# Kernel tuning notes

Measured on AMD Instinct MI355X. Metric: run time of the kernel, lower is better.

The kernel has to match this reference:

```python
import jax, jax.numpy as jnp
import numpy as np

B = 1024
D = 128  # in_out_dim


def _lin(k, i, o):
    return jax.random.normal(k, (i, o), jnp.float32) / np.sqrt(i)


def setup_inputs() -> dict:
    key = jax.random.key(0)
    ks = jax.random.split(key, 24)
    inp = {
        'pseudo_t': jax.random.uniform(ks[0], (), jnp.float32),
        'x': jax.random.normal(ks[1], (B, D), jnp.float32),
        'g_x': jax.random.normal(ks[2], (B, 1), jnp.float32),
        'p': jax.random.uniform(ks[3], (B, 1), jnp.float32),
        # GRN encoder: 128->1024->960->896 (Tanh), decoder 896->128
        'gw0': _lin(ks[4], 128, 1024), 'gb0': jnp.zeros((1024,), jnp.float32),
        'gw1': _lin(ks[5], 1024, 960), 'gb1': jnp.zeros((960,), jnp.float32),
        'gw2': _lin(ks[6], 960, 896), 'gb2': jnp.zeros((896,), jnp.float32),
        'gdw': _lin(ks[7], 896, 128), 'gdb': jnp.zeros((128,), jnp.float32),
        # BRD encoder: 129->512->448 (Tanh), decoder 448->1
        'bw0': _lin(ks[8], 129, 512), 'bb0': jnp.zeros((512,), jnp.float32),
        'bw1': _lin(ks[9], 512, 448), 'bb1': jnp.zeros((448,), jnp.float32),
        'bdw': _lin(ks[10], 448, 1), 'bdb': jnp.zeros((1,), jnp.float32),
    }
    return inp


def reference(pseudo_t, x, g_x, p, gw0, gb0, gw1, gb1, gw2, gb2, gdw, gdb,
              bw0, bb0, bw1, bb1, bdw, bdb):
    bsz = x.shape[0]
    x_gene = x[:, :-1]                       # [B, D-1]
    s = jnp.full((bsz, 1), pseudo_t, x.dtype)

    def grn(state):                          # [..., D] -> [..., D]
        h = jnp.tanh(state @ gw0 + gb0)
        h = jnp.tanh(h @ gw1 + gb1)
        h = jnp.tanh(h @ gw2 + gb2)
        return h @ gdw + gdb

    dx_dt = grn(jnp.concatenate([s, x_gene], axis=1))   # [B, D]

    # BRD growth function g(x, t)
    st = jnp.concatenate([s, x], axis=1)                # [B, D+1]
    e = jnp.tanh(st @ bw0 + bb0)
    e = jnp.tanh(e @ bw1 + bb1)
    g = e @ bdw + bdb                                   # [B, 1]

    # trace of d(dx_dt[:, :D-1]) / d(x_gene), per sample (CNF divergence)
    s_scalar = jnp.reshape(pseudo_t, (1,)).astype(x.dtype)

    def f_single(xg_i):                                 # [D-1] -> [D]
        return grn(jnp.concatenate([s_scalar, xg_i]))

    jac = jax.vmap(jax.jacfwd(f_single))(x_gene)        # [B, D, D-1]
    tr = jnp.trace(jac[:, :D - 1, :], axis1=1, axis2=2) # [B]

    dp_dt = g - p * tr[:, None]                         # [B, 1]
    return (dx_dt, g, dp_dt)
```

## Files before the change

kernel.cpp:

```cpp
#include <hip/hip_runtime.h>


typedef __bf16 bf16;
typedef __bf16 bf16x8 __attribute__((ext_vector_type(8)));
typedef float floatx4 __attribute__((ext_vector_type(4)));

#if defined(__has_builtin)
#if __has_builtin(__builtin_amdgcn_global_load_lds)
#define HAVE_GLL 1
#endif
#endif

typedef __attribute__((address_space(3))) char lds_char_t;
typedef __attribute__((address_space(1))) const char gbl_char_t;

__device__ inline void async_load16(const void* gp, void* lp) {
#ifdef HAVE_GLL
  __builtin_amdgcn_global_load_lds((gbl_char_t*)gp, (lds_char_t*)lp, 16, 0, 0);
#else
  *(bf16x8*)lp = *(const bf16x8*)gp;
#endif
}

__device__ inline void stage_async(const bf16* src, long row0, int ld, int kc,
                                   bf16* dst, int wid, int sr8, int cph) {
#pragma unroll
  for (int t = 0; t < 4; ++t) {
    const int r = (wid * 4 + t) * 8 + sr8;
    const int csrc = (cph - r) & 7;
    async_load16(src + (row0 + r) * (size_t)ld + kc + csrc * 8,
                 dst + r * 64 + cph * 8);
  }
}

__device__ inline void mfma_block(const bf16* As, const bf16* Bs,
                                  floatx4 (&acc)[4][4], int wm, int wn,
                                  int l16, int quad) {
#pragma unroll
  for (int ks = 0; ks < 2; ++ks) {
    bf16x8 af[4], bfv[4];
#pragma unroll
    for (int mt = 0; mt < 4; ++mt) {
      const int r = wm * 64 + mt * 16 + l16;
      const int c = (ks * 4 + quad + r) & 7;
      af[mt] = *(const bf16x8*)(As + r * 64 + c * 8);
    }
#pragma unroll
    for (int nt = 0; nt < 4; ++nt) {
      const int r = wn * 64 + nt * 16 + l16;
      const int c = (ks * 4 + quad + r) & 7;
      bfv[nt] = *(const bf16x8*)(Bs + r * 64 + c * 8);
    }
#pragma unroll
    for (int mt = 0; mt < 4; ++mt)
#pragma unroll
      for (int nt = 0; nt < 4; ++nt)
        acc[mt][nt] = __builtin_amdgcn_mfma_f32_16x16x32_bf16(af[mt], bfv[nt], acc[mt][nt], 0, 0, 0);
  }
}

__device__ inline void g0_body(bf16* G0, const bf16* gw0b, const bf16* d0b,
                               int i0, int ch, int b, int tid) {
  const int nb = ((b >> 9) << 3) + (b & 7);
  const int inner = (b >> 3) & 63;
  if (nb >= ch) return;
  const int e = inner * 256 + tid;
  const int d = e >> 7;
  const int j = (e & 127) << 3;
  const int ig = i0 + nb;
  const int wsel = (d + 1 < 128) ? d + 1 : 127;
  bf16x8 gv = *(const bf16x8*)(gw0b + wsel * 1024 + j);
  bf16x8 dv = *(const bf16x8*)(d0b + (size_t)ig * 1024 + j);
  bf16x8 v;
#pragma unroll
  for (int k = 0; k < 8; ++k) v[k] = (bf16)((float)gv[k] * (float)dv[k]);
  *(bf16x8*)(G0 + ((size_t)nb * 128 + d) * 1024 + j) = v;
}

struct TArgs {
  const bf16* A;
  const bf16* B;
  const bf16* d1b;
  bf16* Upr;
  const bf16* d2b;
  const float* gdw;
  float* tr;
  int i0; int K; int ch;
};

__global__ __launch_bounds__(256, 4) void kt_b1(TArgs p) {
  const int idx = blockIdx.x;
  const int mt8 = (idx >> 3) & 7;
  const int nb  = ((idx >> 6) << 3) + (idx & 7);
  if (nb >= p.ch) return;

  __shared__ __align__(16) char lds[34816];
  bf16* As = (bf16*)lds;
  bf16* Bs = As + 8192;
  bf16* bounce = (bf16*)lds;

  const int tid  = threadIdx.x;
  const int wid  = tid >> 6, lane = tid & 63;
  const int wm   = wid & 1, wn = wid >> 1;
  const int quad = lane >> 4, l16 = lane & 15;
  const int sr8  = lane >> 3, cph = lane & 7;
  const int m0   = mt8 * 128;
  const int ig   = p.i0 + nb;
  const int n0   = nb * 128;

  floatx4 acc[4][4];
#pragma unroll
  for (int a = 0; a < 4; ++a)
#pragma unroll
    for (int b = 0; b < 4; ++b)
#pragma unroll
      for (int r = 0; r < 4; ++r) acc[a][b][r] = 0.0f;

  for (int kc = 0; kc < p.K; kc += 64) {
    stage_async(p.A, m0, 1024, kc, As, wid, sr8, cph);
    stage_async(p.B, n0, 1024, kc, Bs, wid, sr8, cph);
    __syncthreads();
    mfma_block(As, Bs, acc, wm, wn, l16, quad);
    __syncthreads();
  }

#pragma unroll
  for (int nt = 0; nt < 4; ++nt) {
    const int nl = wn * 64 + nt * 16 + l16;
#pragma unroll
    for (int mt = 0; mt < 4; ++mt)
#pragma unroll
      for (int r = 0; r < 4; ++r) {
        const int ml = wm * 64 + mt * 16 + quad * 4 + r;
        const int mg = m0 + ml;
        const float d1v = (mg < 960) ? (float)p.d1b[(size_t)ig * 960 + mg] : 0.0f;
        bounce[nl * 136 + ml] = (bf16)(acc[mt][nt][r] * d1v);
      }
  }
  __syncthreads();
  const int r2 = tid >> 1, half16 = tid & 1;
  const int chLim = (mt8 == 7) ? 8 : 16;
#pragma unroll
  for (int c = 0; c < 8; ++c) {
    const int ch16 = half16 * 8 + c;
    if (ch16 < chLim) {
      bf16x8 v = *(const bf16x8*)(bounce + r2 * 136 + ch16 * 8);
      *(bf16x8*)(p.Upr + (size_t)(n0 + r2) * 1024 + m0 + ch16 * 8) = v;
    }
  }
}

__global__ __launch_bounds__(256, 4) void kt_b2g0(TArgs p, int nB2,
                                                  bf16* G0n, const bf16* gw0b,
                                                  const bf16* d0b, int i0n, int chn) {
  __shared__ __align__(16) char lds[34816];
  __shared__ float red4[4];
  const int tid = threadIdx.x;
  const int idx = blockIdx.x;

  if (idx >= nB2) {
    if (chn > 0) g0_body(G0n, gw0b, d0b, i0n, chn, idx - nB2, tid);
    return;
  }

  const int mt8 = (idx >> 3) & 7;
  const int nb  = ((idx >> 6) << 3) + (idx & 7);
  if (nb >= p.ch || mt8 == 7) return;

  bf16* As = (bf16*)lds;
  bf16* Bs = As + 8192;

  const int wid  = tid >> 6, lane = tid & 63;
  const int wm   = wid & 1, wn = wid >> 1;
  const int quad = lane >> 4, l16 = lane & 15;
  const int sr8  = lane >> 3, cph = lane & 7;
  const int m0   = mt8 * 128;
  const int ig   = p.i0 + nb;
  const int n0   = nb * 128;

  floatx4 acc[4][4];
#pragma unroll
  for (int a = 0; a < 4; ++a)
#pragma unroll
    for (int b = 0; b < 4; ++b)
#pragma unroll
      for (int r = 0; r < 4; ++r) acc[a][b][r] = 0.0f;

  for (int kc = 0; kc < p.K; kc += 64) {
    stage_async(p.A, m0, 1024, kc, As, wid, sr8, cph);
    stage_async(p.B, n0, 1024, kc, Bs, wid, sr8, cph);
    __syncthreads();
    mfma_block(As, Bs, acc, wm, wn, l16, quad);
    __syncthreads();
  }

  float s = 0.0f;
#pragma unroll
  for (int nt = 0; nt < 4; ++nt) {
    const int d = wn * 64 + nt * 16 + l16;
    if (d < 127) {
#pragma unroll
      for (int mt = 0; mt < 4; ++mt)
#pragma unroll
        for (int r = 0; r < 4; ++r) {
          const int mg = m0 + wm * 64 + mt * 16 + quad * 4 + r;
          const float w = (float)p.d2b[(size_t)ig * 896 + mg] * p.gdw[mg * 128 + d];
          s += acc[mt][nt][r] * w;
        }
    }
  }
#pragma unroll
  for (int off = 1; off < 64; off <<= 1) s += __shfl_xor(s, off, 64);
  if (lane == 0) red4[wid] = s;
  __syncthreads();
  if (tid == 0) atomicAdd(p.tr + ig, red4[0] + red4[1] + red4[2] + red4[3]);
}

struct FArgs {
  const bf16* A; int lda;
  const bf16* Bt; int ldb;
  const float* bias;
  bf16* C; int ldc;
  bf16* D; int ldd;
  float* outF; int ldo;
  int K; int realN; int gridX;
};

template <int ACT>
__device__ inline void fwd_body(const FArgs& p, int bx, bf16* As, bf16* Bs) {
  const int tid  = threadIdx.x;
  const int wid  = tid >> 6, lane = tid & 63;
  const int wm   = wid & 1, wn = wid >> 1;
  const int quad = lane >> 4, l16 = lane & 15;
  const int sr8  = lane >> 3, cph = lane & 7;
  const int m0   = (bx % p.gridX) * 128;
  const int bn0  = (bx / p.gridX) * 128;

  floatx4 acc[4][4];
#pragma unroll
  for (int a = 0; a < 4; ++a)
#pragma unroll
    for (int b = 0; b < 4; ++b)
#pragma unroll
      for (int r = 0; r < 4; ++r) acc[a][b][r] = 0.0f;

  for (int kc = 0; kc < p.K; kc += 64) {
    stage_async(p.A, m0, p.lda, kc, As, wid, sr8, cph);
    stage_async(p.Bt, bn0, p.ldb, kc, Bs, wid, sr8, cph);
    __syncthreads();
    mfma_block(As, Bs, acc, wm, wn, l16, quad);
    __syncthreads();
  }

#pragma unroll
  for (int nt = 0; nt < 4; ++nt) {
    const int ng = bn0 + wn * 64 + nt * 16 + l16;
    const float bv = (ng < p.realN) ? p.bias[ng] : 0.0f;
#pragma unroll
    for (int mt = 0; mt < 4; ++mt)
#pragma unroll
      for (int r = 0; r < 4; ++r) {
        const int i = m0 + wm * 64 + mt * 16 + quad * 4 + r;
        const float v = acc[mt][nt][r] + bv;
        if (ACT) {
          const float t = tanhf(v);
          p.C[(size_t)i * p.ldc + ng] = (ng < p.realN) ? (bf16)t : (bf16)0.0f;
          if (p.D && ng < p.realN)
            p.D[(size_t)i * p.ldd + ng] = (bf16)(1.0f - t * t);
        } else if (ng < p.realN) {
          p.outF[(size_t)i * p.ldo + ng] = v;
        }
      }
  }
}

__global__ __launch_bounds__(256) void kt_fwd2(FArgs a, int na, FArgs b) {
  __shared__ __align__(16) bf16 As[8192];
  __shared__ __align__(16) bf16 Bs[8192];
  const int bx = blockIdx.x;
  if (bx < na) fwd_body<1>(a, bx, As, Bs);
  else         fwd_body<1>(b, bx - na, As, Bs);
}

__global__ __launch_bounds__(256) void kt_l2g0(FArgs a, int na, bf16* G0,
                                               const bf16* gw0b, const bf16* d0b,
                                               int i0, int ch) {
  __shared__ __align__(16) bf16 As[8192];
  __shared__ __align__(16) bf16 Bs[8192];
  const int bx = blockIdx.x;
  if (bx < na) fwd_body<1>(a, bx, As, Bs);
  else         g0_body(G0, gw0b, d0b, i0, ch, bx - na, threadIdx.x);
}

__global__ __launch_bounds__(256) void kt_dxgdot(FArgs a, int na,
                                                 const bf16* e1b, const float* bdw,
                                                 const float* bdb, float* gf,
                                                 float* gout) {
  __shared__ __align__(16) bf16 As[8192];
  __shared__ __align__(16) bf16 Bs[8192];
  const int bx = blockIdx.x;
  if (bx < na) { fwd_body<0>(a, bx, As, Bs); return; }
  const int i = (bx - na) * 4 + (threadIdx.x >> 6);
  const int lane = threadIdx.x & 63;
  float s = 0.0f;
  for (int k = lane; k < 448; k += 64) s += (float)e1b[(size_t)i * 512 + k] * bdw[k];
#pragma unroll
  for (int off = 32; off > 0; off >>= 1) s += __shfl_down(s, off, 64);
  if (lane == 0) {
    const float v = s + bdb[0];
    gf[i] = v;
    gout[i] = v;
  }
}

struct PArgs {
  const float *gw0, *gw1, *gw2, *gdw, *bw0, *bw1, *pt, *x;
  bf16 *gw0b, *gw0t, *gw1t, *gw2t, *gdwt, *bw0t, *bw1t, *Xg, *Xb;
};

__device__ inline void tpose_tile(bf16* dst, const float* src, int R, int C,
                                  int ldd, int tile, int tilesX, float* tl,
                                  int tid) {
  const int r0 = (tile % tilesX) * 64;
  const int c0 = (tile / tilesX) * 64;
  const int tx = tid & 63, ty0 = tid >> 6;
#pragma unroll
  for (int i = 0; i < 16; ++i) {
    const int ty = ty0 + i * 4;
    const int r = r0 + ty, c = c0 + tx;
    tl[ty * 65 + tx] = (r < R && c < C) ? src[(size_t)r * C + c] : 0.0f;
  }
  __syncthreads();
#pragma unroll
  for (int i = 0; i < 16; ++i) {
    const int ty = ty0 + i * 4;
    dst[(size_t)(c0 + ty) * ldd + r0 + tx] = (bf16)tl[tx * 65 + ty];
  }
}

__global__ __launch_bounds__(256) void kt_prep(PArgs p) {
  __shared__ float tl[64 * 65];
  int b = blockIdx.x;
  const int t = threadIdx.x;
  if (b < 512) { p.gw0b[b * 256 + t] = (bf16)p.gw0[b * 256 + t]; return; }
  b -= 512;
  if (b < 768) {
    const int idx = b * 256 + t;
    const int i = idx / 192, c = idx % 192;
    const float s = p.pt[0];
    float vb;
    if (c == 0) vb = s;
    else if (c <= 128) vb = p.x[i * 128 + c - 1];
    else vb = 0.0f;
    p.Xb[i * 192 + c] = (bf16)vb;
    if (c < 128) p.Xg[i * 128 + c] = (bf16)((c == 0) ? s : p.x[i * 128 + c - 1]);
    return;
  }
  b -= 768;
  if (b < 32)  { tpose_tile(p.gw0t, p.gw0, 128, 1024, 128, b, 2, tl, t);  return; }
  b -= 32;
  if (b < 256) { tpose_tile(p.gw1t, p.gw1, 1024, 960, 1024, b, 16, tl, t); return; }
  b -= 256;
  if (b < 256) { tpose_tile(p.gw2t, p.gw2, 960, 896, 1024, b, 16, tl, t); return; }
  b -= 256;
  if (b < 32)  { tpose_tile(p.gdwt, p.gdw, 896, 128, 1024, b, 16, tl, t); return; }
  b -= 32;
  if (b < 24)  { tpose_tile(p.bw0t, p.bw0, 129, 512, 192, b, 3, tl, t);  return; }
  b -= 24;
  if (b < 64)  { tpose_tile(p.bw1t, p.bw1, 512, 448, 512, b, 8, tl, t);  return; }
}

__global__ __launch_bounds__(256) void kt_fin(const float* gf, const float* tr,
                                              const float* pp, float* dp) {
  const int i = blockIdx.x * 256 + threadIdx.x;
  if (i < 1024) dp[i] = gf[i] - pp[i] * tr[i];
}

extern "C" void kernel_launch(void* const* d_in, const int* in_sizes, int n_in,
                              void* d_out, int out_size, void* d_ws, size_t ws_size,
                              hipStream_t stream) {
  const float* pt  = (const float*)d_in[0];
  const float* x   = (const float*)d_in[1];
  const float* pp  = (const float*)d_in[3];
  const float* gw0 = (const float*)d_in[4];
  const float* gb0 = (const float*)d_in[5];
  const float* gw1 = (const float*)d_in[6];
  const float* gb1 = (const float*)d_in[7];
  const float* gw2 = (const float*)d_in[8];
  const float* gb2 = (const float*)d_in[9];
  const float* gdw = (const float*)d_in[10];
  const float* gdb = (const float*)d_in[11];
  const float* bw0 = (const float*)d_in[12];
  const float* bb0 = (const float*)d_in[13];
  const float* bw1 = (const float*)d_in[14];
  const float* bb1 = (const float*)d_in[15];
  const float* bdw = (const float*)d_in[16];
  const float* bdb = (const float*)d_in[17];
  float* out = (float*)d_out;

  char* w = (char*)d_ws;
  size_t used = 0;
  auto alloc = [&](size_t nbytes) -> void* {
    void* r = w + used;
    used += (nbytes + 255) & ~(size_t)255;
    return r;
  };
  bf16* gw0b = (bf16*)alloc((size_t)128 * 1024 * 2);
  bf16* gw0t = (bf16*)alloc((size_t)1024 * 128 * 2);
  bf16* gw1t = (bf16*)alloc((size_t)1024 * 1024 * 2);
  bf16* gw2t = (bf16*)alloc((size_t)1024 * 1024 * 2);
  bf16* gdwt = (bf16*)alloc((size_t)128 * 1024 * 2);
  bf16* bw0t = (bf16*)alloc((size_t)512 * 192 * 2);
  bf16* bw1t = (bf16*)alloc((size_t)512 * 512 * 2);
  bf16* Xg   = (bf16*)alloc((size_t)1024 * 128 * 2);
  bf16* Xb   = (bf16*)alloc((size_t)1024 * 192 * 2);
  bf16* h0b  = (bf16*)alloc((size_t)1024 * 1024 * 2);
  bf16* h1b  = (bf16*)alloc((size_t)1024 * 1024 * 2);
  bf16* h2b  = (bf16*)alloc((size_t)1024 * 1024 * 2);
  bf16* e0b  = (bf16*)alloc((size_t)1024 * 512 * 2);
  bf16* e1b  = (bf16*)alloc((size_t)1024 * 512 * 2);
  bf16* d0b  = (bf16*)alloc((size_t)1024 * 1024 * 2);
  bf16* d1b  = (bf16*)alloc((size_t)1024 * 960 * 2);
  bf16* d2b  = (bf16*)alloc((size_t)1024 * 896 * 2);
  float* gf  = (float*)alloc(1024 * 4);
  float* tr  = (float*)alloc(1024 * 4);

  const size_t perSample = (size_t)128 * 1024 * 2;
  size_t avail = (ws_size > used) ? ws_size - used : 0;
  int CH = (int)(avail / (2 * perSample));
  if (CH > 256) CH = 256;
  if (CH < 1) CH = 1;
  bf16* G0  = (bf16*)alloc((size_t)CH * perSample);
  bf16* Upr = (bf16*)(w + used);

  hipMemsetAsync(tr, 0, 1024 * 4, stream);

  {
    PArgs a{gw0, gw1, gw2, gdw, bw0, bw1, pt, x,
            gw0b, gw0t, gw1t, gw2t, gdwt, bw0t, bw1t, Xg, Xb};
    kt_prep<<<dim3(1944), 256, 0, stream>>>(a);
  }

  {
    FArgs a{}; a.A = Xg; a.lda = 128; a.Bt = gw0t; a.ldb = 128; a.bias = gb0;
    a.C = h0b; a.ldc = 1024; a.D = d0b; a.ldd = 1024; a.K = 128; a.realN = 1024;
    a.gridX = 8;
    FArgs b{}; b.A = Xb; b.lda = 192; b.Bt = bw0t; b.ldb = 192; b.bias = bb0;
    b.C = e0b; b.ldc = 512; b.K = 192; b.realN = 512; b.gridX = 8;
    kt_fwd2<<<dim3(96), 256, 0, stream>>>(a, 64, b);
  }
  {
    FArgs a{}; a.A = h0b; a.lda = 1024; a.Bt = gw1t; a.ldb = 1024; a.bias = gb1;
    a.C = h1b; a.ldc = 1024; a.D = d1b; a.ldd = 960; a.K = 1024; a.realN = 960;
    a.gridX = 8;
    FArgs b{}; b.A = e0b; b.lda = 512; b.Bt = bw1t; b.ldb = 512; b.bias = bb1;
    b.C = e1b; b.ldc = 512; b.K = 512; b.realN = 448; b.gridX = 8;
    kt_fwd2<<<dim3(96), 256, 0, stream>>>(a, 64, b);
  }
  const int ch0  = (1024 < CH) ? 1024 : CH;
  const int ch08 = (ch0 + 7) & ~7;
  {
    FArgs a{}; a.A = h1b; a.lda = 1024; a.Bt = gw2t; a.ldb = 1024; a.bias = gb2;
    a.C = h2b; a.ldc = 1024; a.D = d2b; a.ldd = 896; a.K = 1024; a.realN = 896;
    a.gridX = 8;
    kt_l2g0<<<dim3(56 + ch08 * 64), 256, 0, stream>>>(a, 56, G0, gw0b, d0b, 0, ch0);
  }
  {
    FArgs a{}; a.A = h2b; a.lda = 1024; a.Bt = gdwt; a.ldb = 1024; a.bias = gdb;
    a.outF = out; a.ldo = 128; a.K = 896; a.realN = 128; a.gridX = 8;
    kt_dxgdot<<<dim3(8 + 256), 256, 0, stream>>>(a, 8, e1b, bdw, bdb, gf, out + 131072);
  }

  for (int i0 = 0; i0 < 1024; i0 += CH) {
    const int ch  = (1024 - i0 < CH) ? (1024 - i0) : CH;
    const int ch8 = (ch + 7) & ~7;
    {
      TArgs a{}; a.A = gw1t; a.B = G0; a.d1b = d1b; a.Upr = Upr; a.i0 = i0;
      a.K = 1024; a.ch = ch;
      kt_b1<<<dim3(8 * ch8), 256, 0, stream>>>(a);
    }
    {
      const int i0n = i0 + CH;
      const int chn = (i0n < 1024) ? ((1024 - i0n < CH) ? (1024 - i0n) : CH) : 0;
      const int chn8 = (chn + 7) & ~7;
      TArgs a{}; a.A = gw2t; a.B = Upr; a.d2b = d2b; a.gdw = gdw; a.tr = tr;
      a.i0 = i0; a.K = 960; a.ch = ch;
      kt_b2g0<<<dim3(8 * ch8 + chn8 * 64), 256, 0, stream>>>(
          a, 8 * ch8, G0, gw0b, d0b, i0n, chn);
    }
  }

  kt_fin<<<dim3(4), 256, 0, stream>>>(gf, tr, pp, out + 132096);
}
```

Before: 840.4 us.

## Replace Jacobian GEMM kernels with 256x256-tile double-buffered pipelined MFMA kernels

The two per-chunk Jacobian GEMMs move from 128x128 tiles with 256 threads and a synchronous single-buffer K loop to 256x256 tiles with 512 threads. The new K loop uses 128KB of dynamic LDS, a double-buffered async global-to-LDS prefetch with swizzled layout, explicit vmcnt waits and setprio around the MFMA bursts. The epilogue writes directly to global memory instead of bouncing through LDS. The next-chunk G0 construction changes from extra appended blocks to a grid-stride loop run by all GEMM blocks after their tile. This targets higher arithmetic intensity and overlap of loads with MFMA, at the cost of fewer resident blocks and wave-quantization effects on the larger tiles.

```diff
diff --git a/kernel.cpp b/kernel.cpp
--- a/kernel.cpp
+++ b/kernel.cpp
@@ -77,143 +77,221 @@
   *(bf16x8*)(G0 + ((size_t)nb * 128 + d) * 1024 + j) = v;
 }
 
-struct TArgs {
+struct T8 {
   const bf16* A;
-  const bf16* B;
-  const bf16* d1b;
+  const bf16* Bm;
+  const bf16* sc;
   bf16* Upr;
-  const bf16* d2b;
   const float* gdw;
   float* tr;
-  int i0; int K; int ch;
+  int i0, NT, ch, nTiles;
+  int chn, i0n;
+  bf16* G0;
+  const bf16* gw0b;
+  const bf16* d0b;
 };
 
-__global__ __launch_bounds__(256, 4) void kt_b1(TArgs p) {
-  const int idx = blockIdx.x;
-  const int mt8 = (idx >> 3) & 7;
-  const int nb  = ((idx >> 6) << 3) + (idx & 7);
-  if (nb >= p.ch) return;
-
-  __shared__ __align__(16) char lds[34816];
-  bf16* As = (bf16*)lds;
-  bf16* Bs = As + 8192;
-  bf16* bounce = (bf16*)lds;
-
-  const int tid  = threadIdx.x;
-  const int wid  = tid >> 6, lane = tid & 63;
-  const int wm   = wid & 1, wn = wid >> 1;
+__device__ __forceinline__ void gemm256(const bf16* Aop, const bf16* Bop,
+                                        int m0, int n0, int NT, char* lds,
+                                        floatx4 (&acc)[8][4]) {
+  const int tid = threadIdx.x;
+  const int wid = tid >> 6, lane = tid & 63;
+  const int wm = wid & 1, wn = wid >> 1;
   const int quad = lane >> 4, l16 = lane & 15;
-  const int sr8  = lane >> 3, cph = lane & 7;
-  const int m0   = mt8 * 128;
-  const int ig   = p.i0 + nb;
-  const int n0   = nb * 128;
-
-  floatx4 acc[4][4];
-#pragma unroll
-  for (int a = 0; a < 4; ++a)
+
+  const int sr = tid >> 2;
+  const int sg = tid & 3;
+  const int gs = sg ^ (sr & 3);
+  const bf16* aS0 = Aop + (size_t)(m0 + sr) * 1024 + gs * 8;
+  const bf16* aS1 = aS0 + (size_t)128 * 1024;
+  const bf16* bS0 = Bop + (size_t)(n0 + sr) * 1024 + gs * 8;
+  const bf16* bS1 = bS0 + (size_t)128 * 1024;
+  const int dO0 = tid * 16, dO1 = 8192 + tid * 16;
+
+  const int fsw = (quad ^ (l16 & 3)) * 8;
+  const int fo  = (wm * 128 + l16) * 32 + fsw;
+  const int fob = (wn * 64  + l16) * 32 + fsw;
+
+#define STAGE_PAIR(tt, ss)                                                     \
+  {                                                                            \
+    char* db = lds + (((tt) & 1) * 65536) + ((ss) * 16384);                    \
+    const int kc = (tt) * 64 + (ss) * 32;                                      \
+    async_load16(aS0 + kc, db + dO0);                                          \
+    async_load16(aS1 + kc, db + dO1);                                          \
+    async_load16(bS0 + kc, db + 32768 + dO0);                                  \
+    async_load16(bS1 + kc, db + 32768 + dO1);                                  \
+  }
+
+#define PHASE(T, S, DOSTAGE, ST, SS, VMSEL)                                    \
+  {                                                                            \
+    const bf16* Af = (const bf16*)(lds + ((T) & 1) * 65536 + (S) * 16384) + fo;\
+    const bf16* Bf = (const bf16*)(lds + ((T) & 1) * 65536 + 32768 +           \
+                                   (S) * 16384) + fob;                         \
+    bf16x8 af[8], bv[4];                                                       \
+    _Pragma("unroll")                                                          \
+    for (int mf = 0; mf < 8; ++mf) af[mf] = *(const bf16x8*)(Af + mf * 512);   \
+    _Pragma("unroll")                                                          \
+    for (int nf = 0; nf < 4; ++nf) bv[nf] = *(const bf16x8*)(Bf + nf * 512);   \
+    if (DOSTAGE) STAGE_PAIR(ST, SS);                                           \
+    __builtin_amdgcn_sched_barrier(0);                                         \
+    {                                                                          \
+      const int vms = (VMSEL);                                                 \
+      if (vms == 8)      asm volatile("s_waitcnt vmcnt(8)");                   \
+      else if (vms == 4) asm volatile("s_waitcnt vmcnt(4)");                   \
+      else if (vms == 0) asm volatile("s_waitcnt vmcnt(0)");                   \
+    }                                                                          \
+    __builtin_amdgcn_sched_barrier(0);                                         \
+    __builtin_amdgcn_s_setprio(1);                                             \
+    _Pragma("unroll")                                                          \
+    for (int mf = 0; mf < 8; ++mf)                                             \
+      _Pragma("unroll")                                                        \
+      for (int nf = 0; nf < 4; ++nf)                                           \
+        acc[mf][nf] = __builtin_amdgcn_mfma_f32_16x16x32_bf16(                 \
+            af[mf], bv[nf], acc[mf][nf], 0, 0, 0);                             \
+    __builtin_amdgcn_s_setprio(0);                                             \
+    asm volatile("s_waitcnt lgkmcnt(0)");                                      \
+    __builtin_amdgcn_sched_barrier(0);                                         \
+    __builtin_amdgcn_s_barrier();                                              \
+    __builtin_amdgcn_sched_barrier(0);                                         \
+  }
+
+  STAGE_PAIR(0, 0);
+  STAGE_PAIR(0, 1);
+  STAGE_PAIR(1, 0);
+  __builtin_amdgcn_sched_barrier(0);
+  asm volatile("s_waitcnt vmcnt(8)");
+  __builtin_amdgcn_sched_barrier(0);
+  __builtin_amdgcn_s_barrier();
+  __builtin_amdgcn_sched_barrier(0);
+
+#pragma unroll 2
+  for (int t = 0; t < NT; ++t) {
+    PHASE(t, 0, (t + 1 < NT), t + 1, 1, (t + 1 < NT) ? 8 : 0);
+    PHASE(t, 1, (t + 2 < NT), t + 2, 0,
+          (t + 2 < NT) ? 8 : ((t + 1 < NT) ? 4 : -1));
+  }
+#undef PHASE
+#undef STAGE_PAIR
+}
+
+__global__ __launch_bounds__(512, 2) void kt8_b1(T8 p) {
+  extern __shared__ __align__(16) char lds[];
+  const int mt = (blockIdx.x >> 3) & 3;
+  const int nt = ((blockIdx.x >> 5) << 3) | (blockIdx.x & 7);
+  if (nt >= p.nTiles) return;
+
+  floatx4 acc[8][4];
+#pragma unroll
+  for (int a = 0; a < 8; ++a)
 #pragma unroll
     for (int b = 0; b < 4; ++b)
 #pragma unroll
       for (int r = 0; r < 4; ++r) acc[a][b][r] = 0.0f;
 
-  for (int kc = 0; kc < p.K; kc += 64) {
-    stage_async(p.A, m0, 1024, kc, As, wid, sr8, cph);
-    stage_async(p.B, n0, 1024, kc, Bs, wid, sr8, cph);
+  gemm256(p.A, p.Bm, mt * 256, nt * 256, p.NT, lds, acc);
+
+  const int tid = threadIdx.x;
+  const int wid = tid >> 6, lane = tid & 63;
+  const int wm = wid & 1, wn = wid >> 1;
+  const int quad = lane >> 4, l16 = lane & 15;
+  const long nLim = (long)p.ch * 128;
+  const int mb = mt * 256 + wm * 128;
+
+#pragma unroll
+  for (int nf = 0; nf < 4; ++nf) {
+    const long n = (long)nt * 256 + wn * 64 + nf * 16 + l16;
+    if (n < nLim) {
+      const int ig = p.i0 + (int)(n >> 7);
+      const bf16* dp = p.sc + (size_t)ig * 960;
+      bf16* urow = p.Upr + (size_t)n * 1024;
+#pragma unroll
+      for (int mf = 0; mf < 8; ++mf) {
+        const int mg = mb + mf * 16 + quad * 4;
+        if (mg < 960) {
+          union { bf16 h[4]; uint2 u; } o;
+#pragma unroll
+          for (int r = 0; r < 4; ++r)
+            o.h[r] = (bf16)(acc[mf][nf][r] * (float)dp[mg + r]);
+          *(uint2*)(urow + mg) = o.u;
+        }
+      }
+    }
+  }
+}
+
+__global__ __launch_bounds__(512, 2) void kt8_b2(T8 p) {
+  extern __shared__ __align__(16) char lds[];
+  const int mt = (blockIdx.x >> 3) & 3;
+  const int nt = ((blockIdx.x >> 5) << 3) | (blockIdx.x & 7);
+  const int tid = threadIdx.x;
+
+  if (nt < p.nTiles) {
+    floatx4 acc[8][4];
+#pragma unroll
+    for (int a = 0; a < 8; ++a)
+#pragma unroll
+      for (int b = 0; b < 4; ++b)
+#pragma unroll
+        for (int r = 0; r < 4; ++r) acc[a][b][r] = 0.0f;
+
+    gemm256(p.A, p.Bm, mt * 256, nt * 256, p.NT, lds, acc);
+
+    const int wid = tid >> 6, lane = tid & 63;
+    const int wm = wid & 1, wn = wid >> 1;
+    const int quad = lane >> 4, l16 = lane & 15;
+    const long nLim = (long)p.ch * 128;
+    const int mb = mt * 256 + wm * 128;
+
+    float s = 0.0f;
+#pragma unroll
+    for (int nf = 0; nf < 4; ++nf) {
+      const long n = (long)nt * 256 + wn * 64 + nf * 16 + l16;
+      const int d = (int)(n & 127);
+      if (n < nLim && d < 127) {
+        const int ig = p.i0 + (int)(n >> 7);
+        const bf16* dp = p.sc + (size_t)ig * 896;
+#pragma unroll
+        for (int mf = 0; mf < 8; ++mf) {
+          const int mg = mb + mf * 16 + quad * 4;
+          if (mg < 896) {
+#pragma unroll
+            for (int r = 0; r < 4; ++r) {
+              const float w = (float)dp[mg + r] * p.gdw[(mg + r) * 128 + d];
+              s += acc[mf][nf][r] * w;
+            }
+          }
+        }
+      }
+    }
+#pragma unroll
+    for (int off = 1; off < 64; off <<= 1) s += __shfl_xor(s, off, 64);
+    float* red = (float*)lds;
+    if (lane == 0) red[wid] = s;
     __syncthreads();
-    mfma_block(As, Bs, acc, wm, wn, l16, quad);
-    __syncthreads();
-  }
-
-#pragma unroll
-  for (int nt = 0; nt < 4; ++nt) {
-    const int nl = wn * 64 + nt * 16 + l16;
-#pragma unroll
-    for (int mt = 0; mt < 4; ++mt)
-#pragma unroll
-      for (int r = 0; r < 4; ++r) {
-        const int ml = wm * 64 + mt * 16 + quad * 4 + r;
-        const int mg = m0 + ml;
-        const float d1v = (mg < 960) ? (float)p.d1b[(size_t)ig * 960 + mg] : 0.0f;
-        bounce[nl * 136 + ml] = (bf16)(acc[mt][nt][r] * d1v);
-      }
-  }
-  __syncthreads();
-  const int r2 = tid >> 1, half16 = tid & 1;
-  const int chLim = (mt8 == 7) ? 8 : 16;
-#pragma unroll
-  for (int c = 0; c < 8; ++c) {
-    const int ch16 = half16 * 8 + c;
-    if (ch16 < chLim) {
-      bf16x8 v = *(const bf16x8*)(bounce + r2 * 136 + ch16 * 8);
-      *(bf16x8*)(p.Upr + (size_t)(n0 + r2) * 1024 + m0 + ch16 * 8) = v;
-    }
-  }
-}
-
-__global__ __launch_bounds__(256, 4) void kt_b2g0(TArgs p, int nB2,
-                                                  bf16* G0n, const bf16* gw0b,
-                                                  const bf16* d0b, int i0n, int chn) {
-  __shared__ __align__(16) char lds[34816];
-  __shared__ float red4[4];
-  const int tid = threadIdx.x;
-  const int idx = blockIdx.x;
-
-  if (idx >= nB2) {
-    if (chn > 0) g0_body(G0n, gw0b, d0b, i0n, chn, idx - nB2, tid);
-    return;
-  }
-
-  const int mt8 = (idx >> 3) & 7;
-  const int nb  = ((idx >> 6) << 3) + (idx & 7);
-  if (nb >= p.ch || mt8 == 7) return;
-
-  bf16* As = (bf16*)lds;
-  bf16* Bs = As + 8192;
-
-  const int wid  = tid >> 6, lane = tid & 63;
-  const int wm   = wid & 1, wn = wid >> 1;
-  const int quad = lane >> 4, l16 = lane & 15;
-  const int sr8  = lane >> 3, cph = lane & 7;
-  const int m0   = mt8 * 128;
-  const int ig   = p.i0 + nb;
-  const int n0   = nb * 128;
-
-  floatx4 acc[4][4];
-#pragma unroll
-  for (int a = 0; a < 4; ++a)
-#pragma unroll
-    for (int b = 0; b < 4; ++b)
-#pragma unroll
-      for (int r = 0; r < 4; ++r) acc[a][b][r] = 0.0f;
-
-  for (int kc = 0; kc < p.K; kc += 64) {
-    stage_async(p.A, m0, 1024, kc, As, wid, sr8, cph);
-    stage_async(p.B, n0, 1024, kc, Bs, wid, sr8, cph);
-    __syncthreads();
-    mfma_block(As, Bs, acc, wm, wn, l16, quad);
-    __syncthreads();
-  }
-
-  float s = 0.0f;
-#pragma unroll
-  for (int nt = 0; nt < 4; ++nt) {
-    const int d = wn * 64 + nt * 16 + l16;
-    if (d < 127) {
-#pragma unroll
-      for (int mt = 0; mt < 4; ++mt)
-#pragma unroll
-        for (int r = 0; r < 4; ++r) {
-          const int mg = m0 + wm * 64 + mt * 16 + quad * 4 + r;
-          const float w = (float)p.d2b[(size_t)ig * 896 + mg] * p.gdw[mg * 128 + d];
-          s += acc[mt][nt][r] * w;
-        }
-    }
-  }
-#pragma unroll
-  for (int off = 1; off < 64; off <<= 1) s += __shfl_xor(s, off, 64);
-  if (lane == 0) red4[wid] = s;
-  __syncthreads();
-  if (tid == 0) atomicAdd(p.tr + ig, red4[0] + red4[1] + red4[2] + red4[3]);
+    const int igA = p.i0 + nt * 2;
+    if (tid == 0)
+      atomicAdd(p.tr + igA, red[0] + red[1] + red[2] + red[3]);
+    if (tid == 256 && nt * 2 + 1 < p.ch)
+      atomicAdd(p.tr + igA + 1, red[4] + red[5] + red[6] + red[7]);
+  }
+
+  if (p.chn > 0) {
+    const size_t V = (size_t)p.chn * 16384;
+    for (size_t v = (size_t)blockIdx.x * 512 + tid; v < V;
+         v += (size_t)gridDim.x * 512) {
+      const int j = ((int)(v & 127)) << 3;
+      const size_t rest = v >> 7;
+      const int d = (int)(rest & 127);
+      const int nb = (int)(rest >> 7);
+      const int wsel = (d + 1 < 128) ? d + 1 : 127;
+      bf16x8 gv = *(const bf16x8*)(p.gw0b + wsel * 1024 + j);
+      bf16x8 dv = *(const bf16x8*)(p.d0b + (size_t)(p.i0n + nb) * 1024 + j);
+      bf16x8 o;
+#pragma unroll
+      for (int k = 0; k < 8; ++k) o[k] = (bf16)((float)gv[k] * (float)dv[k]);
+      *(bf16x8*)(p.G0 + ((size_t)nb * 128 + d) * 1024 + j) = o;
+    }
+  }
 }
 
 struct FArgs {
@@ -397,6 +475,15 @@
   const float* bdw = (const float*)d_in[16];
   const float* bdb = (const float*)d_in[17];
   float* out = (float*)d_out;
+
+  static bool s_attr = false;
+  if (!s_attr) {
+    hipFuncSetAttribute((const void*)kt8_b1,
+                        hipFuncAttributeMaxDynamicSharedMemorySize, 131072);
+    hipFuncSetAttribute((const void*)kt8_b2,
+                        hipFuncAttributeMaxDynamicSharedMemorySize, 131072);
+    s_attr = true;
+  }
 
   char* w = (char*)d_ws;
   size_t used = 0;
@@ -429,6 +516,7 @@
   size_t avail = (ws_size > used) ? ws_size - used : 0;
   int CH = (int)(avail / (2 * perSample));
   if (CH > 256) CH = 256;
+  if (CH >= 2) CH &= ~1;
   if (CH < 1) CH = 1;
   bf16* G0  = (bf16*)alloc((size_t)CH * perSample);
   bf16* Upr = (bf16*)(w + used);
@@ -473,20 +561,20 @@
 
   for (int i0 = 0; i0 < 1024; i0 += CH) {
     const int ch  = (1024 - i0 < CH) ? (1024 - i0) : CH;
-    const int ch8 = (ch + 7) & ~7;
+    const int nTiles = (ch * 128 + 255) >> 8;
+    const int nT8 = (nTiles + 7) & ~7;
     {
-      TArgs a{}; a.A = gw1t; a.B = G0; a.d1b = d1b; a.Upr = Upr; a.i0 = i0;
-      a.K = 1024; a.ch = ch;
-      kt_b1<<<dim3(8 * ch8), 256, 0, stream>>>(a);
+      T8 a{}; a.A = gw1t; a.Bm = G0; a.sc = d1b; a.Upr = Upr; a.i0 = i0;
+      a.NT = 16; a.ch = ch; a.nTiles = nTiles;
+      kt8_b1<<<dim3(nT8 * 4), 512, 131072, stream>>>(a);
     }
     {
       const int i0n = i0 + CH;
       const int chn = (i0n < 1024) ? ((1024 - i0n < CH) ? (1024 - i0n) : CH) : 0;
-      const int chn8 = (chn + 7) & ~7;
-      TArgs a{}; a.A = gw2t; a.B = Upr; a.d2b = d2b; a.gdw = gdw; a.tr = tr;
-      a.i0 = i0; a.K = 960; a.ch = ch;
-      kt_b2g0<<<dim3(8 * ch8 + chn8 * 64), 256, 0, stream>>>(
-          a, 8 * ch8, G0, gw0b, d0b, i0n, chn);
+      T8 a{}; a.A = gw2t; a.Bm = Upr; a.sc = d2b; a.gdw = gdw; a.tr = tr;
+      a.i0 = i0; a.NT = 15; a.ch = ch; a.nTiles = nTiles;
+      a.chn = chn; a.i0n = i0n; a.G0 = G0; a.gw0b = gw0b; a.d0b = d0b;
+      kt8_b2<<<dim3(nT8 * 4), 512, 131072, stream>>>(a);
     }
   }
 
```

Result: faster. 805.0 us (-4.2%).

## Fuse G0 construction into B1 staging and software-pipeline B1/B2 chunks

Applied to the files above, without the earlier changes.

Removes the materialized G0 buffer by computing the gw0·d0 product on the fly while staging the B operand of the first Jacobian GEMM. Merges the B1 GEMM of chunk c+1 and the B2 GEMM of chunk c into a single launch, using double-buffered Upr workspaces so the two stages overlap and there are fewer launches. The chunk size is rounded down to a power of two. This saves G0 global writes and reads but replaces async global-to-LDS loads with synchronous register loads plus multiplies. It also uses more workspace per chunk, which may shrink the chunk size.

```diff
diff --git a/kernel.cpp b/kernel.cpp
--- a/kernel.cpp
+++ b/kernel.cpp
@@ -33,6 +33,23 @@
   }
 }
 
+__device__ inline void stage_b_otf(const bf16* w0b, const bf16* d0row, int kc,
+                                   bf16* dst, int wid, int sr8, int cph) {
+#pragma unroll
+  for (int t = 0; t < 4; ++t) {
+    const int r = (wid * 4 + t) * 8 + sr8;
+    const int csrc = (cph - r) & 7;
+    const int wsel = (r + 1 < 128) ? r + 1 : 127;
+    const int off = kc + csrc * 8;
+    bf16x8 wv = *(const bf16x8*)(w0b + wsel * 1024 + off);
+    bf16x8 dv = *(const bf16x8*)(d0row + off);
+    bf16x8 o;
+#pragma unroll
+    for (int k = 0; k < 8; ++k) o[k] = (bf16)((float)wv[k] * (float)dv[k]);
+    *(bf16x8*)(dst + r * 64 + cph * 8) = o;
+  }
+}
+
 __device__ inline void mfma_block(const bf16* As, const bf16* Bs,
                                   floatx4 (&acc)[4][4], int wm, int wn,
                                   int l16, int quad) {
@@ -59,45 +76,30 @@
   }
 }
 
-__device__ inline void g0_body(bf16* G0, const bf16* gw0b, const bf16* d0b,
-                               int i0, int ch, int b, int tid) {
-  const int nb = ((b >> 9) << 3) + (b & 7);
-  const int inner = (b >> 3) & 63;
-  if (nb >= ch) return;
-  const int e = inner * 256 + tid;
-  const int d = e >> 7;
-  const int j = (e & 127) << 3;
-  const int ig = i0 + nb;
-  const int wsel = (d + 1 < 128) ? d + 1 : 127;
-  bf16x8 gv = *(const bf16x8*)(gw0b + wsel * 1024 + j);
-  bf16x8 dv = *(const bf16x8*)(d0b + (size_t)ig * 1024 + j);
-  bf16x8 v;
-#pragma unroll
-  for (int k = 0; k < 8; ++k) v[k] = (bf16)((float)gv[k] * (float)dv[k]);
-  *(bf16x8*)(G0 + ((size_t)nb * 128 + d) * 1024 + j) = v;
-}
-
-struct TArgs {
-  const bf16* A;
-  const bf16* B;
+struct T12 {
+  const bf16* A1;
+  const bf16* w0b;
+  const bf16* d0b;
   const bf16* d1b;
-  bf16* Upr;
+  bf16* UprW;
+  int i0b1;
+  const bf16* A2;
+  const bf16* UprR;
   const bf16* d2b;
   const float* gdw;
   float* tr;
-  int i0; int K; int ch;
+  int i0b2;
+  int ch;
 };
 
-__global__ __launch_bounds__(256, 4) void kt_b1(TArgs p) {
-  const int idx = blockIdx.x;
+__device__ inline void b1_body(const T12& p, int idx, char* ldsRaw) {
   const int mt8 = (idx >> 3) & 7;
   const int nb  = ((idx >> 6) << 3) + (idx & 7);
   if (nb >= p.ch) return;
 
-  __shared__ __align__(16) char lds[34816];
-  bf16* As = (bf16*)lds;
+  bf16* As = (bf16*)ldsRaw;
   bf16* Bs = As + 8192;
-  bf16* bounce = (bf16*)lds;
+  bf16* bounce = (bf16*)ldsRaw;
 
   const int tid  = threadIdx.x;
   const int wid  = tid >> 6, lane = tid & 63;
@@ -105,8 +107,9 @@
   const int quad = lane >> 4, l16 = lane & 15;
   const int sr8  = lane >> 3, cph = lane & 7;
   const int m0   = mt8 * 128;
-  const int ig   = p.i0 + nb;
+  const int ig   = p.i0b1 + nb;
   const int n0   = nb * 128;
+  const bf16* d0row = p.d0b + (size_t)ig * 1024;
 
   floatx4 acc[4][4];
 #pragma unroll
@@ -116,9 +119,9 @@
 #pragma unroll
       for (int r = 0; r < 4; ++r) acc[a][b][r] = 0.0f;
 
-  for (int kc = 0; kc < p.K; kc += 64) {
-    stage_async(p.A, m0, 1024, kc, As, wid, sr8, cph);
-    stage_async(p.B, n0, 1024, kc, Bs, wid, sr8, cph);
+  for (int kc = 0; kc < 1024; kc += 64) {
+    stage_async(p.A1, m0, 1024, kc, As, wid, sr8, cph);
+    stage_b_otf(p.w0b, d0row, kc, Bs, wid, sr8, cph);
     __syncthreads();
     mfma_block(As, Bs, acc, wm, wn, l16, quad);
     __syncthreads();
@@ -145,37 +148,27 @@
     const int ch16 = half16 * 8 + c;
     if (ch16 < chLim) {
       bf16x8 v = *(const bf16x8*)(bounce + r2 * 136 + ch16 * 8);
-      *(bf16x8*)(p.Upr + (size_t)(n0 + r2) * 1024 + m0 + ch16 * 8) = v;
+      *(bf16x8*)(p.UprW + (size_t)(n0 + r2) * 1024 + m0 + ch16 * 8) = v;
     }
   }
 }
 
-__global__ __launch_bounds__(256, 4) void kt_b2g0(TArgs p, int nB2,
-                                                  bf16* G0n, const bf16* gw0b,
-                                                  const bf16* d0b, int i0n, int chn) {
-  __shared__ __align__(16) char lds[34816];
-  __shared__ float red4[4];
-  const int tid = threadIdx.x;
-  const int idx = blockIdx.x;
-
-  if (idx >= nB2) {
-    if (chn > 0) g0_body(G0n, gw0b, d0b, i0n, chn, idx - nB2, tid);
-    return;
-  }
-
+__device__ inline void b2_body(const T12& p, int idx, char* ldsRaw,
+                               float* red4) {
   const int mt8 = (idx >> 3) & 7;
   const int nb  = ((idx >> 6) << 3) + (idx & 7);
   if (nb >= p.ch || mt8 == 7) return;
 
-  bf16* As = (bf16*)lds;
+  bf16* As = (bf16*)ldsRaw;
   bf16* Bs = As + 8192;
 
+  const int tid  = threadIdx.x;
   const int wid  = tid >> 6, lane = tid & 63;
   const int wm   = wid & 1, wn = wid >> 1;
   const int quad = lane >> 4, l16 = lane & 15;
   const int sr8  = lane >> 3, cph = lane & 7;
   const int m0   = mt8 * 128;
-  const int ig   = p.i0 + nb;
+  const int ig   = p.i0b2 + nb;
   const int n0   = nb * 128;
 
   floatx4 acc[4][4];
@@ -186,9 +179,9 @@
 #pragma unroll
       for (int r = 0; r < 4; ++r) acc[a][b][r] = 0.0f;
 
-  for (int kc = 0; kc < p.K; kc += 64) {
-    stage_async(p.A, m0, 1024, kc, As, wid, sr8, cph);
-    stage_async(p.B, n0, 1024, kc, Bs, wid, sr8, cph);
+  for (int kc = 0; kc < 960; kc += 64) {
+    stage_async(p.A2, m0, 1024, kc, As, wid, sr8, cph);
+    stage_async(p.UprR, n0, 1024, kc, Bs, wid, sr8, cph);
     __syncthreads();
     mfma_block(As, Bs, acc, wm, wn, l16, quad);
     __syncthreads();
@@ -214,6 +207,22 @@
   if (lane == 0) red4[wid] = s;
   __syncthreads();
   if (tid == 0) atomicAdd(p.tr + ig, red4[0] + red4[1] + red4[2] + red4[3]);
+}
+
+__global__ __launch_bounds__(256, 4) void kt_b12(T12 p, int nB2, int nB1) {
+  __shared__ __align__(16) char lds[34816];
+  __shared__ float red4[4];
+  const int bid = blockIdx.x;
+  int sel, idx;
+  if (nB2 > 0 && nB1 > 0) {
+    sel = (bid >> 3) & 1;
+    idx = ((bid >> 4) << 3) | (bid & 7);
+  } else {
+    sel = (nB2 > 0) ? 0 : 1;
+    idx = bid;
+  }
+  if (sel == 0) b2_body(p, idx, lds, red4);
+  else          b1_body(p, idx, lds);
 }
 
 struct FArgs {
@@ -282,14 +291,10 @@
   else         fwd_body<1>(b, bx - na, As, Bs);
 }
 
-__global__ __launch_bounds__(256) void kt_l2g0(FArgs a, int na, bf16* G0,
-                                               const bf16* gw0b, const bf16* d0b,
-                                               int i0, int ch) {
+__global__ __launch_bounds__(256) void kt_fwd1(FArgs a) {
   __shared__ __align__(16) bf16 As[8192];
   __shared__ __align__(16) bf16 Bs[8192];
-  const int bx = blockIdx.x;
-  if (bx < na) fwd_body<1>(a, bx, As, Bs);
-  else         g0_body(G0, gw0b, d0b, i0, ch, bx - na, threadIdx.x);
+  fwd_body<1>(a, blockIdx.x, As, Bs);
 }
 
 __global__ __launch_bounds__(256) void kt_dxgdot(FArgs a, int na,
@@ -429,9 +434,12 @@
   size_t avail = (ws_size > used) ? ws_size - used : 0;
   int CH = (int)(avail / (2 * perSample));
   if (CH > 256) CH = 256;
+  while (CH & (CH - 1)) CH &= CH - 1;
   if (CH < 1) CH = 1;
-  bf16* G0  = (bf16*)alloc((size_t)CH * perSample);
-  bf16* Upr = (bf16*)(w + used);
+  bf16* UprA = (bf16*)alloc((size_t)CH * perSample);
+  bf16* UprB = (bf16*)alloc((size_t)CH * perSample);
+  const int nCh = 1024 / CH;
+  const int ch8 = (CH + 7) & ~7;
 
   hipMemsetAsync(tr, 0, 1024 * 4, stream);
 
@@ -457,13 +465,11 @@
     b.C = e1b; b.ldc = 512; b.K = 512; b.realN = 448; b.gridX = 8;
     kt_fwd2<<<dim3(96), 256, 0, stream>>>(a, 64, b);
   }
-  const int ch0  = (1024 < CH) ? 1024 : CH;
-  const int ch08 = (ch0 + 7) & ~7;
   {
     FArgs a{}; a.A = h1b; a.lda = 1024; a.Bt = gw2t; a.ldb = 1024; a.bias = gb2;
     a.C = h2b; a.ldc = 1024; a.D = d2b; a.ldd = 896; a.K = 1024; a.realN = 896;
     a.gridX = 8;
-    kt_l2g0<<<dim3(56 + ch08 * 64), 256, 0, stream>>>(a, 56, G0, gw0b, d0b, 0, ch0);
+    kt_fwd1<<<dim3(56), 256, 0, stream>>>(a);
   }
   {
     FArgs a{}; a.A = h2b; a.lda = 1024; a.Bt = gdwt; a.ldb = 1024; a.bias = gdb;
@@ -471,23 +477,24 @@
     kt_dxgdot<<<dim3(8 + 256), 256, 0, stream>>>(a, 8, e1b, bdw, bdb, gf, out + 131072);
   }
 
-  for (int i0 = 0; i0 < 1024; i0 += CH) {
-    const int ch  = (1024 - i0 < CH) ? (1024 - i0) : CH;
-    const int ch8 = (ch + 7) & ~7;
-    {
-      TArgs a{}; a.A = gw1t; a.B = G0; a.d1b = d1b; a.Upr = Upr; a.i0 = i0;
-      a.K = 1024; a.ch = ch;
-      kt_b1<<<dim3(8 * ch8), 256, 0, stream>>>(a);
-    }
-    {
-      const int i0n = i0 + CH;
-      const int chn = (i0n < 1024) ? ((1024 - i0n < CH) ? (1024 - i0n) : CH) : 0;
-      const int chn8 = (chn + 7) & ~7;
-      TArgs a{}; a.A = gw2t; a.B = Upr; a.d2b = d2b; a.gdw = gdw; a.tr = tr;
-      a.i0 = i0; a.K = 960; a.ch = ch;
-      kt_b2g0<<<dim3(8 * ch8 + chn8 * 64), 256, 0, stream>>>(
-          a, 8 * ch8, G0, gw0b, d0b, i0n, chn);
-    }
+  {
+    T12 a{};
+    a.A1 = gw1t; a.w0b = gw0b; a.d0b = d0b; a.d1b = d1b;
+    a.UprW = UprA; a.i0b1 = 0; a.ch = CH;
+    kt_b12<<<dim3(8 * ch8), 256, 0, stream>>>(a, 0, 8 * ch8);
+  }
+  for (int c = 0; c < nCh; ++c) {
+    bf16* uprCur = (c & 1) ? UprB : UprA;
+    bf16* uprNxt = (c & 1) ? UprA : UprB;
+    const int nB2 = 8 * ch8;
+    const int nB1 = (c + 1 < nCh) ? 8 * ch8 : 0;
+    T12 a{};
+    a.A2 = gw2t; a.UprR = uprCur; a.d2b = d2b; a.gdw = gdw; a.tr = tr;
+    a.i0b2 = c * CH;
+    a.A1 = gw1t; a.w0b = gw0b; a.d0b = d0b; a.d1b = d1b;
+    a.UprW = uprNxt; a.i0b1 = (c + 1) * CH;
+    a.ch = CH;
+    kt_b12<<<dim3(nB2 + nB1), 256, 0, stream>>>(a, nB2, nB1);
   }
 
   kt_fin<<<dim3(4), 256, 0, stream>>>(gf, tr, pp, out + 132096);
```

Result: slower. 911.0 us (+8.4%).

## Compute tangent G0 on the fly in kt_b1 staging instead of materializing it

Applied to the files above, without the earlier changes.

Drops the separate G0 buffer (the per-sample diag(d0)·W0 tangent matrix) and the g0_body blocks that wrote it. kt_b1 now builds its B tile directly in LDS from gw0b rows and the sample's d0 row. This removes a large global write/read round trip and frees workspace so the sample chunk can be larger. In exchange, B staging becomes synchronous register loads plus multiplies instead of async global-to-LDS copies, which may reduce load/compute overlap.

```diff
diff --git a/kernel.cpp b/kernel.cpp
--- a/kernel.cpp
+++ b/kernel.cpp
@@ -33,6 +33,23 @@
   }
 }
 
+__device__ inline void stage_b_otf(const bf16* w0b, const bf16* d0row, int kc,
+                                   bf16* dst, int wid, int sr8, int cph) {
+#pragma unroll
+  for (int t = 0; t < 4; ++t) {
+    const int r = (wid * 4 + t) * 8 + sr8;
+    const int csrc = (cph - r) & 7;
+    const int wsel = (r + 1 < 128) ? r + 1 : 127;
+    const int off = kc + csrc * 8;
+    bf16x8 wv = *(const bf16x8*)(w0b + wsel * 1024 + off);
+    bf16x8 dv = *(const bf16x8*)(d0row + off);
+    bf16x8 o;
+#pragma unroll
+    for (int k = 0; k < 8; ++k) o[k] = (bf16)((float)wv[k] * (float)dv[k]);
+    *(bf16x8*)(dst + r * 64 + cph * 8) = o;
+  }
+}
+
 __device__ inline void mfma_block(const bf16* As, const bf16* Bs,
                                   floatx4 (&acc)[4][4], int wm, int wn,
                                   int l16, int quad) {
@@ -59,33 +76,16 @@
   }
 }
 
-__device__ inline void g0_body(bf16* G0, const bf16* gw0b, const bf16* d0b,
-                               int i0, int ch, int b, int tid) {
-  const int nb = ((b >> 9) << 3) + (b & 7);
-  const int inner = (b >> 3) & 63;
-  if (nb >= ch) return;
-  const int e = inner * 256 + tid;
-  const int d = e >> 7;
-  const int j = (e & 127) << 3;
-  const int ig = i0 + nb;
-  const int wsel = (d + 1 < 128) ? d + 1 : 127;
-  bf16x8 gv = *(const bf16x8*)(gw0b + wsel * 1024 + j);
-  bf16x8 dv = *(const bf16x8*)(d0b + (size_t)ig * 1024 + j);
-  bf16x8 v;
-#pragma unroll
-  for (int k = 0; k < 8; ++k) v[k] = (bf16)((float)gv[k] * (float)dv[k]);
-  *(bf16x8*)(G0 + ((size_t)nb * 128 + d) * 1024 + j) = v;
-}
-
 struct TArgs {
   const bf16* A;
-  const bf16* B;
+  const bf16* w0b;
+  const bf16* d0b;
   const bf16* d1b;
   bf16* Upr;
   const bf16* d2b;
   const float* gdw;
   float* tr;
-  int i0; int K; int ch;
+  int i0; int ch;
 };
 
 __global__ __launch_bounds__(256, 4) void kt_b1(TArgs p) {
@@ -107,6 +107,7 @@
   const int m0   = mt8 * 128;
   const int ig   = p.i0 + nb;
   const int n0   = nb * 128;
+  const bf16* d0row = p.d0b + (size_t)ig * 1024;
 
   floatx4 acc[4][4];
 #pragma unroll
@@ -116,9 +117,9 @@
 #pragma unroll
       for (int r = 0; r < 4; ++r) acc[a][b][r] = 0.0f;
 
-  for (int kc = 0; kc < p.K; kc += 64) {
+  for (int kc = 0; kc < 1024; kc += 64) {
     stage_async(p.A, m0, 1024, kc, As, wid, sr8, cph);
-    stage_async(p.B, n0, 1024, kc, Bs, wid, sr8, cph);
+    stage_b_otf(p.w0b, d0row, kc, Bs, wid, sr8, cph);
     __syncthreads();
     mfma_block(As, Bs, acc, wm, wn, l16, quad);
     __syncthreads();
@@ -150,26 +151,18 @@
   }
 }
 
-__global__ __launch_bounds__(256, 4) void kt_b2g0(TArgs p, int nB2,
-                                                  bf16* G0n, const bf16* gw0b,
-                                                  const bf16* d0b, int i0n, int chn) {
-  __shared__ __align__(16) char lds[34816];
-  __shared__ float red4[4];
-  const int tid = threadIdx.x;
+__global__ __launch_bounds__(256, 4) void kt_b2(TArgs p) {
   const int idx = blockIdx.x;
-
-  if (idx >= nB2) {
-    if (chn > 0) g0_body(G0n, gw0b, d0b, i0n, chn, idx - nB2, tid);
-    return;
-  }
-
   const int mt8 = (idx >> 3) & 7;
   const int nb  = ((idx >> 6) << 3) + (idx & 7);
   if (nb >= p.ch || mt8 == 7) return;
 
+  __shared__ __align__(16) char lds[34816];
+  __shared__ float red4[4];
   bf16* As = (bf16*)lds;
   bf16* Bs = As + 8192;
 
+  const int tid  = threadIdx.x;
   const int wid  = tid >> 6, lane = tid & 63;
   const int wm   = wid & 1, wn = wid >> 1;
   const int quad = lane >> 4, l16 = lane & 15;
@@ -186,9 +179,9 @@
 #pragma unroll
       for (int r = 0; r < 4; ++r) acc[a][b][r] = 0.0f;
 
-  for (int kc = 0; kc < p.K; kc += 64) {
+  for (int kc = 0; kc < 960; kc += 64) {
     stage_async(p.A, m0, 1024, kc, As, wid, sr8, cph);
-    stage_async(p.B, n0, 1024, kc, Bs, wid, sr8, cph);
+    stage_async(p.Upr, n0, 1024, kc, Bs, wid, sr8, cph);
     __syncthreads();
     mfma_block(As, Bs, acc, wm, wn, l16, quad);
     __syncthreads();
@@ -282,14 +275,10 @@
   else         fwd_body<1>(b, bx - na, As, Bs);
 }
 
-__global__ __launch_bounds__(256) void kt_l2g0(FArgs a, int na, bf16* G0,
-                                               const bf16* gw0b, const bf16* d0b,
-                                               int i0, int ch) {
+__global__ __launch_bounds__(256) void kt_fwd1(FArgs a) {
   __shared__ __align__(16) bf16 As[8192];
   __shared__ __align__(16) bf16 Bs[8192];
-  const int bx = blockIdx.x;
-  if (bx < na) fwd_body<1>(a, bx, As, Bs);
-  else         g0_body(G0, gw0b, d0b, i0, ch, bx - na, threadIdx.x);
+  fwd_body<1>(a, blockIdx.x, As, Bs);
 }
 
 __global__ __launch_bounds__(256) void kt_dxgdot(FArgs a, int na,
@@ -427,10 +416,9 @@
 
   const size_t perSample = (size_t)128 * 1024 * 2;
   size_t avail = (ws_size > used) ? ws_size - used : 0;
-  int CH = (int)(avail / (2 * perSample));
+  int CH = (int)(avail / perSample);
   if (CH > 256) CH = 256;
   if (CH < 1) CH = 1;
-  bf16* G0  = (bf16*)alloc((size_t)CH * perSample);
   bf16* Upr = (bf16*)(w + used);
 
   hipMemsetAsync(tr, 0, 1024 * 4, stream);
@@ -457,13 +445,11 @@
     b.C = e1b; b.ldc = 512; b.K = 512; b.realN = 448; b.gridX = 8;
     kt_fwd2<<<dim3(96), 256, 0, stream>>>(a, 64, b);
   }
-  const int ch0  = (1024 < CH) ? 1024 : CH;
-  const int ch08 = (ch0 + 7) & ~7;
   {
     FArgs a{}; a.A = h1b; a.lda = 1024; a.Bt = gw2t; a.ldb = 1024; a.bias = gb2;
     a.C = h2b; a.ldc = 1024; a.D = d2b; a.ldd = 896; a.K = 1024; a.realN = 896;
     a.gridX = 8;
-    kt_l2g0<<<dim3(56 + ch08 * 64), 256, 0, stream>>>(a, 56, G0, gw0b, d0b, 0, ch0);
+    kt_fwd1<<<dim3(56), 256, 0, stream>>>(a);
   }
   {
     FArgs a{}; a.A = h2b; a.lda = 1024; a.Bt = gdwt; a.ldb = 1024; a.bias = gdb;
@@ -475,18 +461,14 @@
     const int ch  = (1024 - i0 < CH) ? (1024 - i0) : CH;
     const int ch8 = (ch + 7) & ~7;
     {
-      TArgs a{}; a.A = gw1t; a.B = G0; a.d1b = d1b; a.Upr = Upr; a.i0 = i0;
-      a.K = 1024; a.ch = ch;
+      TArgs a{}; a.A = gw1t; a.w0b = gw0b; a.d0b = d0b; a.d1b = d1b;
+      a.Upr = Upr; a.i0 = i0; a.ch = ch;
       kt_b1<<<dim3(8 * ch8), 256, 0, stream>>>(a);
     }
     {
-      const int i0n = i0 + CH;
-      const int chn = (i0n < 1024) ? ((1024 - i0n < CH) ? (1024 - i0n) : CH) : 0;
-      const int chn8 = (chn + 7) & ~7;
-      TArgs a{}; a.A = gw2t; a.B = Upr; a.d2b = d2b; a.gdw = gdw; a.tr = tr;
-      a.i0 = i0; a.K = 960; a.ch = ch;
-      kt_b2g0<<<dim3(8 * ch8 + chn8 * 64), 256, 0, stream>>>(
-          a, 8 * ch8, G0, gw0b, d0b, i0n, chn);
+      TArgs a{}; a.A = gw2t; a.Upr = Upr; a.d2b = d2b; a.gdw = gdw; a.tr = tr;
+      a.i0 = i0; a.ch = ch;
+      kt_b2<<<dim3(8 * ch8), 256, 0, stream>>>(a);
     }
   }
 
```

New measurement: 840.4 us. No clear change (+0.0%).
